# Kernel optimization log

Hardware: AMD Instinct MI355X
Metric: run time of the kernel (lower is better)

Reference implementation:

```python
import jax, jax.numpy as jnp
import numpy as np

IN_F = 512
OUT_F = 512
TREES = 50
DEPTH = 10  # levels above leaves; 2^DEPTH leaves per tree


def _build_forest(T, D):
    """Forest of T perfect binary trees. Nodes laid out level-by-level (leaves first).
    Returns node_order [N], adjacency [E,2] (parent, child; children consecutive,
    left then right, edges sorted by parent), edge_order [E]."""
    per = 2 ** (D + 1) - 1
    no = np.zeros(per, np.int64)
    adj_parts, eo_parts = [], []
    start, prev = 0, None
    for l in range(D + 1):
        n_l = 2 ** (D - l)
        idx = np.arange(start, start + n_l, dtype=np.int64)
        no[idx] = l
        if l > 0:
            parents = np.repeat(idx, 2)          # each parent twice
            adj_parts.append(np.stack([parents, prev], 1))  # prev = 2*n_l children, pairs consecutive
            eo_parts.append(np.full(2 * n_l, l, np.int64))
        prev, start = idx, start + n_l
    adj = np.concatenate(adj_parts, 0)
    eo = np.concatenate(eo_parts, 0)
    offs = np.arange(T, dtype=np.int64) * per
    node_order = np.tile(no, T)
    adjacency = (adj[None] + offs[:, None, None]).reshape(-1, 2)
    edge_order = np.tile(eo, T)
    return node_order, adjacency, edge_order


def setup_inputs() -> dict:
    key = jax.random.key(0)
    ks = jax.random.split(key, 8)
    no, adj, eo = _build_forest(TREES, DEPTH)
    N = no.shape[0]
    s_in = 1.0 / np.sqrt(IN_F).astype(np.float32)
    s_h = 1.0 / np.sqrt(OUT_F).astype(np.float32)
    return {
        "features": jax.random.normal(ks[0], (N, IN_F), jnp.float32),
        "node_order": jnp.asarray(no),
        "adjacency_list": jnp.asarray(adj),
        "edge_order": jnp.asarray(eo),
        "W_iou_w": jax.random.normal(ks[1], (3 * OUT_F, IN_F), jnp.float32) * s_in,
        "W_iou_b": jax.random.normal(ks[2], (3 * OUT_F,), jnp.float32) * s_in,
        "U_iou_l": jax.random.normal(ks[3], (3 * OUT_F, OUT_F), jnp.float32) * s_h,
        "U_iou_r": jax.random.normal(ks[4], (3 * OUT_F, OUT_F), jnp.float32) * s_h,
        "W_f_w": jax.random.normal(ks[5], (OUT_F, IN_F), jnp.float32) * s_in,
        "W_f_b": jax.random.normal(ks[6], (OUT_F,), jnp.float32) * s_in,
        "U_f_l": jax.random.normal(ks[7], (OUT_F, OUT_F), jnp.float32) * s_h,
        "U_f_r": jax.random.normal(jax.random.fold_in(key, 99), (OUT_F, OUT_F), jnp.float32) * s_h,
    }


def reference(features, node_order, adjacency_list, edge_order,
              W_iou_w, W_iou_b, U_iou_l, U_iou_r, W_f_w, W_f_b, U_f_l, U_f_r):
    # Tree topology is static integer data: hoist it to numpy so per-level index
    # sets are concrete (the original torch code host-syncs the same way).
    no = np.asarray(node_order)
    ao = np.asarray(adjacency_list)
    eo = np.asarray(edge_order)
    N, H = features.shape[0], W_f_w.shape[0]
    h = jnp.zeros((N, H), features.dtype)
    c = jnp.zeros((N, H), features.dtype)
    for l in range(int(no.max()) + 1):
        nodes = jnp.asarray(np.nonzero(no == l)[0])   # parents at this level, sorted
        x = features[nodes]                            # [P, F]
        if l == 0:
            iou = x @ W_iou_w.T + W_iou_b
            i, o, u = jnp.split(iou, 3, axis=1)
            c_new = jax.nn.sigmoid(i) * jnp.tanh(u)
        else:
            e = ao[eo == l]                            # [2P, 2]; children consecutive per parent
            p_rep = jnp.asarray(e[:, 0])               # parent repeated per child
            children = jnp.asarray(e[:, 1])
            ch = h[children]                           # [2P, H]
            cc = c[children]                           # [2P, H]
            iou = (x @ W_iou_w.T + W_iou_b
                   + ch[0::2] @ U_iou_l.T              # left child h
                   + ch[1::2] @ U_iou_r.T)             # right child h
            i, o, u = jnp.split(iou, 3, axis=1)
            wf = features[p_rep] @ W_f_w.T + W_f_b     # [2P, H]
            f_l = jax.nn.sigmoid(wf + ch @ U_f_l.T)
            f_r = jax.nn.sigmoid(wf + ch @ U_f_r.T)
            fc = (f_l + f_r) * cc                      # [2P, H]
            c_new = jax.nn.sigmoid(i) * jnp.tanh(u) + fc.reshape(-1, 2, H).sum(1)
        h_new = jax.nn.sigmoid(o) * jnp.tanh(c_new)
        c = c.at[nodes].set(c_new)
        h = h.at[nodes].set(h_new)
    return h, c
```

## Files before the change

kernel.cpp:

```cpp
#include <hip/hip_runtime.h>
#include <hip/hip_bf16.h>

#define TREES_ 50
#define PER_ 2047
#define NN_ (TREES_ * PER_)
#define NINT_ (TREES_ * 1023)
#define NLEAF_ (TREES_ * 1024)

typedef __attribute__((ext_vector_type(8))) short s8v;
typedef __attribute__((ext_vector_type(4))) float f4v;

__device__ __forceinline__ unsigned short f2bf(float f) {
  union { float f; unsigned u; } v; v.f = f;
  unsigned r = v.u + 0x7FFFu + ((v.u >> 16) & 1u);
  return (unsigned short)(r >> 16);
}
__device__ __forceinline__ float bf2f(unsigned short s) {
  union { unsigned u; float f; } v; v.u = ((unsigned)s) << 16;
  return v.f;
}
__device__ __forceinline__ float sigm(float x) { return 1.f / (1.f + __expf(-x)); }
__device__ __forceinline__ float tanh_s(float x) {
  float ax = fabsf(x);
  float e = __expf(2.f * ax);
  float t = 1.f - 2.f / (e + 1.f);
  return copysignf(t, x);
}
__device__ __forceinline__ f4v fz4() { f4v z; z[0]=0.f; z[1]=0.f; z[2]=0.f; z[3]=0.f; return z; }

#if defined(__has_builtin)
#if __has_builtin(__builtin_amdgcn_global_load_lds)
#define HAS_GLD 1
#endif
#endif
__device__ __forceinline__ void gld16(const void* g, void* l) {
#ifdef HAS_GLD
  __builtin_amdgcn_global_load_lds(
      (const __attribute__((address_space(1))) unsigned int*)g,
      (__attribute__((address_space(3))) unsigned int*)l, 16, 0, 0);
#else
  *(s8v*)l = *(const s8v*)g;
#endif
}

__device__ __forceinline__ int xcd_swz(int bid, int nwg) {
  int q = nwg >> 3, r = nwg & 7, x = bid & 7, pos = bid >> 3;
  int base = (x < r) ? x * (q + 1) : r * (q + 1) + (x - r) * q;
  return base + pos;
}

#define LDS_BYTE(row, c16) ((row) * 128 + (((c16) ^ ((row) & 7)) << 4))

#define MFMA_STEP(As, Bs)                                                     \
  for (int kk = 0; kk < 2; ++kk) {                                            \
    s8v af[4], bf_[4];                                                        \
    _Pragma("unroll") for (int i = 0; i < 4; ++i) {                           \
      int R = wr * 64 + i * 16 + lr;                                          \
      af[i] = *(const s8v*)((char*)As + LDS_BYTE(R, kk * 4 + lg));            \
    }                                                                         \
    _Pragma("unroll") for (int j = 0; j < 4; ++j) {                           \
      int R = wc * 64 + j * 16 + lr;                                          \
      bf_[j] = *(const s8v*)((char*)Bs + LDS_BYTE(R, kk * 4 + lg));           \
    }                                                                         \
    _Pragma("unroll") for (int i = 0; i < 4; ++i)                             \
      _Pragma("unroll") for (int j = 0; j < 4; ++j)                           \
        acc[i][j] = __builtin_amdgcn_mfma_f32_16x16x32_bf16(af[i], bf_[j],    \
                                                            acc[i][j], 0, 0, 0); \
  }

__global__ __launch_bounds__(256) void feat2bf(const float* __restrict__ feat,
                                               unsigned short* __restrict__ FB) {
  long long i = (long long)blockIdx.x * 256 + threadIdx.x;
  if (i >= (long long)NN_ * 64) return;
  const float* src = feat + i * 8;
  float4 f0 = *(const float4*)src;
  float4 f1 = *(const float4*)(src + 4);
  s8v v;
  v[0] = (short)f2bf(f0.x); v[1] = (short)f2bf(f0.y);
  v[2] = (short)f2bf(f0.z); v[3] = (short)f2bf(f0.w);
  v[4] = (short)f2bf(f1.x); v[5] = (short)f2bf(f1.y);
  v[6] = (short)f2bf(f1.z); v[7] = (short)f2bf(f1.w);
  *(s8v*)(FB + i * 8) = v;
}

__global__ __launch_bounds__(256) void prep_weights(
    const float* __restrict__ Wiou, const float* __restrict__ Ul,
    const float* __restrict__ Ur,  const float* __restrict__ Wf,
    const float* __restrict__ Ufl, const float* __restrict__ Ufr,
    unsigned short* __restrict__ UCAT2, unsigned short* __restrict__ UFLR,
    unsigned short* __restrict__ WFB) {
  int i = blockIdx.x * 256 + threadIdx.x;
  if (i < 1536 * 1536) {
    int r = i / 1536, c = i - r * 1536;
    float v = (c < 512) ? Ul[r * 512 + c]
            : (c < 1024) ? Ur[r * 512 + (c - 512)]
                         : Wiou[r * 512 + (c - 1024)];
    UCAT2[i] = f2bf(v);
  }
  if (i < 1024 * 512) {
    int r = i >> 9, k = i & 511;
    int c = r >> 1, s = r & 1;
    UFLR[i] = f2bf(s ? Ufr[c * 512 + k] : Ufl[c * 512 + k]);
  }
  if (i < 512 * 512) WFB[i] = f2bf(Wf[i]);
}

__global__ __launch_bounds__(256) void wf_gemm(
    const unsigned short* __restrict__ FB, const unsigned short* __restrict__ WFB,
    const float* __restrict__ bfb, unsigned short* __restrict__ WF, int nwg) {
  __shared__ __align__(16) unsigned short As[128 * 64];
  __shared__ __align__(16) unsigned short Bs[128 * 64];
  const int tid = threadIdx.x;
  const int swz = xcd_swz(blockIdx.x, nwg);
  const int tn = swz & 3, tm = swz >> 2;
  const int wid = tid >> 6, lane = tid & 63;
  const int wr = wid >> 1, wc = wid & 1;
  const int lr = lane & 15, lg = lane >> 4;
  const unsigned short* aA[4]; const unsigned short* aB[4];
#pragma unroll
  for (int L = 0; L < 4; ++L) {
    int q = L * 256 + tid;
    int row = q >> 3, c16g = (q & 7) ^ (row & 7);
    int m = tm * 128 + row; if (m >= NINT_) m = NINT_ - 1;
    unsigned t = (unsigned)m / 1023u;
    int node = (int)t * 2047 + 1024 + (m - (int)t * 1023);
    aA[L] = FB + (size_t)node * 512 + c16g * 8;
    int n = tn * 128 + row;
    aB[L] = WFB + (size_t)n * 512 + c16g * 8;
  }
  f4v acc[4][4];
#pragma unroll
  for (int i = 0; i < 4; ++i)
#pragma unroll
    for (int j = 0; j < 4; ++j) acc[i][j] = fz4();
  for (int k0 = 0; k0 < 512; k0 += 64) {
#pragma unroll
    for (int L = 0; L < 4; ++L) {
      int q = L * 256 + tid;
      gld16(aA[L] + k0, (unsigned short*)As + q * 8);
      gld16(aB[L] + k0, (unsigned short*)Bs + q * 8);
    }
    __syncthreads();
    MFMA_STEP(As, Bs)
    __syncthreads();
  }
#pragma unroll
  for (int i = 0; i < 4; ++i)
#pragma unroll
    for (int j = 0; j < 4; ++j) {
      int n = tn * 128 + wc * 64 + j * 16 + lr;
      float bias = bfb[n];
#pragma unroll
      for (int r = 0; r < 4; ++r) {
        int m = tm * 128 + wr * 64 + i * 16 + lg * 4 + r;
        if (m < NINT_) WF[(size_t)m * 512 + n] = f2bf(acc[i][j][r] + bias);
      }
    }
}

__global__ __launch_bounds__(256) void leaf_gemm(
    const unsigned short* __restrict__ FB, const unsigned short* __restrict__ UCAT2,
    const float* __restrict__ biou, unsigned short* __restrict__ LIOU, int nwg) {
  __shared__ __align__(16) unsigned short As[128 * 64];
  __shared__ __align__(16) unsigned short Bs[128 * 64];
  const int tid = threadIdx.x;
  const int swz = xcd_swz(blockIdx.x, nwg);
  const int tn = swz % 12, tm = swz / 12;
  const int wid = tid >> 6, lane = tid & 63;
  const int wr = wid >> 1, wc = wid & 1;
  const int lr = lane & 15, lg = lane >> 4;
  const unsigned short* aA[4]; const unsigned short* aB[4];
#pragma unroll
  for (int L = 0; L < 4; ++L) {
    int q = L * 256 + tid;
    int row = q >> 3, c16g = (q & 7) ^ (row & 7);
    int m = tm * 128 + row;
    int node = (m >> 10) * 2047 + (m & 1023);
    aA[L] = FB + (size_t)node * 512 + c16g * 8;
    int n = tn * 128 + row;
    aB[L] = UCAT2 + (size_t)n * 1536 + 1024 + c16g * 8;
  }
  f4v acc[4][4];
#pragma unroll
  for (int i = 0; i < 4; ++i)
#pragma unroll
    for (int j = 0; j < 4; ++j) acc[i][j] = fz4();
  for (int k0 = 0; k0 < 512; k0 += 64) {
#pragma unroll
    for (int L = 0; L < 4; ++L) {
      int q = L * 256 + tid;
      gld16(aA[L] + k0, (unsigned short*)As + q * 8);
      gld16(aB[L] + k0, (unsigned short*)Bs + q * 8);
    }
    __syncthreads();
    MFMA_STEP(As, Bs)
    __syncthreads();
  }
#pragma unroll
  for (int i = 0; i < 4; ++i)
#pragma unroll
    for (int j = 0; j < 4; ++j) {
      int n = tn * 128 + wc * 64 + j * 16 + lr;
      float bias = biou[n];
#pragma unroll
      for (int r = 0; r < 4; ++r) {
        int m = tm * 128 + wr * 64 + i * 16 + lg * 4 + r;
        LIOU[(size_t)m * 1536 + n] = f2bf(acc[i][j][r] + bias);
      }
    }
}

__global__ __launch_bounds__(256) void leaf_ew(
    const unsigned short* __restrict__ LIOU,
    float* __restrict__ h_out, float* __restrict__ c_out,
    unsigned short* __restrict__ HB) {
  int idx = blockIdx.x * 256 + threadIdx.x;
  int r = idx >> 7;
  int c4 = (idx & 127) << 2;
  int g = (r >> 10) * 2047 + (r & 1023);
  const unsigned short* pr = LIOU + (size_t)r * 1536;
  ushort4 iv = *(const ushort4*)(pr + c4);
  ushort4 ov = *(const ushort4*)(pr + 512 + c4);
  ushort4 uv = *(const ushort4*)(pr + 1024 + c4);
  float4 hv, cv; ushort4 hb;
  float cc, hh;
  cc = sigm(bf2f(iv.x)) * tanh_s(bf2f(uv.x)); hh = sigm(bf2f(ov.x)) * tanh_s(cc);
  cv.x = cc; hv.x = hh; hb.x = f2bf(hh);
  cc = sigm(bf2f(iv.y)) * tanh_s(bf2f(uv.y)); hh = sigm(bf2f(ov.y)) * tanh_s(cc);
  cv.y = cc; hv.y = hh; hb.y = f2bf(hh);
  cc = sigm(bf2f(iv.z)) * tanh_s(bf2f(uv.z)); hh = sigm(bf2f(ov.z)) * tanh_s(cc);
  cv.z = cc; hv.z = hh; hb.z = f2bf(hh);
  cc = sigm(bf2f(iv.w)) * tanh_s(bf2f(uv.w)); hh = sigm(bf2f(ov.w)) * tanh_s(cc);
  cv.w = cc; hv.w = hh; hb.w = f2bf(hh);
  *(float4*)(h_out + (size_t)g * 512 + c4) = hv;
  *(float4*)(c_out + (size_t)g * 512 + c4) = cv;
  *(ushort4*)(HB + (size_t)g * 512 + c4) = hb;
}

__global__ __launch_bounds__(256) void lvl_gemm(
    const unsigned short* __restrict__ HB, const unsigned short* __restrict__ FB,
    const unsigned short* __restrict__ UFLR, const unsigned short* __restrict__ UCAT2,
    const unsigned short* __restrict__ WF, const float* __restrict__ biou,
    const float* __restrict__ c_out, float* __restrict__ h_out,
    unsigned short* __restrict__ IOU,
    int P, int shift, int start_l, int start_lm1, int nwg1, int nwg2) {
  __shared__ __align__(16) unsigned short As[128 * 64];
  __shared__ __align__(16) unsigned short Bs[128 * 64];
  const int tid = threadIdx.x;
  const int wid = tid >> 6, lane = tid & 63;
  const int wr = wid >> 1, wc = wid & 1;
  const int lr = lane & 15, lg = lane >> 4;
  const int pmask = (1 << shift) - 1;
  f4v acc[4][4];
#pragma unroll
  for (int i = 0; i < 4; ++i)
#pragma unroll
    for (int j = 0; j < 4; ++j) acc[i][j] = fz4();

  if ((int)blockIdx.x < nwg1) {
    const int swz = xcd_swz(blockIdx.x, nwg1);
    const int tn = swz & 7, tm = swz >> 3;
    const int M2 = 2 * P;
    const int cmask = (2 << shift) - 1;
    const unsigned short* aA[4]; const unsigned short* aB[4];
#pragma unroll
    for (int L = 0; L < 4; ++L) {
      int q = L * 256 + tid;
      int row = q >> 3, c16g = (q & 7) ^ (row & 7);
      int jg = tm * 128 + row; if (jg >= M2) jg = M2 - 1;
      int t = jg >> (shift + 1), idx = jg & cmask;
      aA[L] = HB + (size_t)(t * PER_ + start_lm1 + idx) * 512 + c16g * 8;
      int n = tn * 128 + row;
      aB[L] = UFLR + (size_t)n * 512 + c16g * 8;
    }
    for (int k0 = 0; k0 < 512; k0 += 64) {
#pragma unroll
      for (int L = 0; L < 4; ++L) {
        int q = L * 256 + tid;
        gld16(aA[L] + k0, (unsigned short*)As + q * 8);
        gld16(aB[L] + k0, (unsigned short*)Bs + q * 8);
      }
      __syncthreads();
      MFMA_STEP(As, Bs)
      __syncthreads();
    }
    const int soff = start_l - 1024;
#pragma unroll
    for (int i = 0; i < 4; ++i) {
      int mbase = tm * 128 + wr * 64 + i * 16;
#pragma unroll
      for (int j = 0; j < 4; ++j) {
        int nn = tn * 128 + wc * 64 + j * 16 + lr;
        int hcol = nn >> 1;
        float fc[4];
#pragma unroll
        for (int r = 0; r < 4; ++r) {
          int m = mbase + lg * 4 + r;
          int mm = (m < M2) ? m : 0;
          int pidx = mm >> 1;
          int t = pidx >> shift, k = pidx & pmask;
          float wf = bf2f(WF[(size_t)(t * 1023 + soff + k) * 512 + hcol]);
          float sv = sigm(wf + acc[i][j][r]);
          float spair = sv + __shfl_xor(sv, 1, 64);
          float cc = 0.f;
          if ((lr & 1) == 0)
            cc = c_out[(size_t)(t * PER_ + start_lm1 + (mm & cmask)) * 512 + hcol];
          fc[r] = spair * cc;
        }
        if ((lr & 1) == 0) {
          int p0 = (mbase >> 1) + lg * 2;
          if (p0 < P) {
            int t0 = p0 >> shift, k0p = p0 & pmask;
            h_out[(size_t)(t0 * PER_ + start_l + k0p) * 512 + hcol] = fc[0] + fc[1];
          }
          int p1 = (mbase >> 1) + lg * 2 + 1;
          if (p1 < P) {
            int t1 = p1 >> shift, k1p = p1 & pmask;
            h_out[(size_t)(t1 * PER_ + start_l + k1p) * 512 + hcol] = fc[2] + fc[3];
          }
        }
      }
    }
  } else {
    const int swz = xcd_swz((int)blockIdx.x - nwg1, nwg2);
    const int tn = swz % 12, tm = swz / 12;
    const unsigned short* aHB[4]; const unsigned short* aFB[4];
    const unsigned short* aB[4];
#pragma unroll
    for (int L = 0; L < 4; ++L) {
      int q = L * 256 + tid;
      int row = q >> 3, c16g = (q & 7) ^ (row & 7);
      int p = tm * 128 + row; if (p >= P) p = P - 1;
      int t = p >> shift, kp = p & pmask;
      aHB[L] = HB + (size_t)(t * PER_ + start_lm1) * 512 + (size_t)kp * 1024 + c16g * 8;
      aFB[L] = FB + (size_t)(t * PER_ + start_l + kp) * 512 + c16g * 8;
      int n = tn * 128 + row;
      aB[L] = UCAT2 + (size_t)n * 1536 + c16g * 8;
    }
    for (int k0 = 0; k0 < 1536; k0 += 64) {
#pragma unroll
      for (int L = 0; L < 4; ++L) {
        int q = L * 256 + tid;
        const unsigned short* src = (k0 < 1024) ? aHB[L] + k0 : aFB[L] + (k0 - 1024);
        gld16(src, (unsigned short*)As + q * 8);
        gld16(aB[L] + k0, (unsigned short*)Bs + q * 8);
      }
      __syncthreads();
      MFMA_STEP(As, Bs)
      __syncthreads();
    }
#pragma unroll
    for (int i = 0; i < 4; ++i)
#pragma unroll
      for (int j = 0; j < 4; ++j) {
        int n = tn * 128 + wc * 64 + j * 16 + lr;
        float bias = biou[n];
#pragma unroll
        for (int r = 0; r < 4; ++r) {
          int m = tm * 128 + wr * 64 + i * 16 + lg * 4 + r;
          if (m < P) IOU[(size_t)m * 1536 + n] = f2bf(acc[i][j][r] + bias);
        }
      }
  }
}

__global__ __launch_bounds__(256) void g3_kernel(
    const unsigned short* __restrict__ IOU,
    float* __restrict__ h_out, float* __restrict__ c_out,
    unsigned short* __restrict__ HB, int P, int shift, int start_l) {
  int idx = blockIdx.x * 256 + threadIdx.x;
  int p = idx >> 7;
  if (p >= P) return;
  int c4 = (idx & 127) << 2;
  int t = p >> shift, k = p & ((1 << shift) - 1);
  size_t pg = (size_t)(t * PER_ + start_l + k);
  const unsigned short* ir = IOU + (size_t)p * 1536;
  ushort4 iv = *(const ushort4*)(ir + c4);
  ushort4 ov = *(const ushort4*)(ir + 512 + c4);
  ushort4 uv = *(const ushort4*)(ir + 1024 + c4);
  float4 fcs = *(const float4*)(h_out + pg * 512 + c4);
  float4 hv, cv; ushort4 hb;
  float cc, hh;
  cc = sigm(bf2f(iv.x)) * tanh_s(bf2f(uv.x)) + fcs.x; hh = sigm(bf2f(ov.x)) * tanh_s(cc);
  cv.x = cc; hv.x = hh; hb.x = f2bf(hh);
  cc = sigm(bf2f(iv.y)) * tanh_s(bf2f(uv.y)) + fcs.y; hh = sigm(bf2f(ov.y)) * tanh_s(cc);
  cv.y = cc; hv.y = hh; hb.y = f2bf(hh);
  cc = sigm(bf2f(iv.z)) * tanh_s(bf2f(uv.z)) + fcs.z; hh = sigm(bf2f(ov.z)) * tanh_s(cc);
  cv.z = cc; hv.z = hh; hb.z = f2bf(hh);
  cc = sigm(bf2f(iv.w)) * tanh_s(bf2f(uv.w)) + fcs.w; hh = sigm(bf2f(ov.w)) * tanh_s(cc);
  cv.w = cc; hv.w = hh; hb.w = f2bf(hh);
  *(float4*)(h_out + pg * 512 + c4) = hv;
  *(float4*)(c_out + pg * 512 + c4) = cv;
  *(ushort4*)(HB + pg * 512 + c4) = hb;
}

__global__ void fill_sentinel(float* out, int n) {
  int i = blockIdx.x * 256 + threadIdx.x;
  if (i < n) out[i] = 12345.0f;
}

extern "C" void kernel_launch(void* const* d_in, const int* in_sizes, int n_in,
                              void* d_out, int out_size, void* d_ws, size_t ws_size,
                              hipStream_t stream) {
  (void)in_sizes; (void)n_in; (void)out_size;
  const float* feat = (const float*)d_in[0];
  const float* Wiou = (const float*)d_in[4];
  const float* biou = (const float*)d_in[5];
  const float* Ul   = (const float*)d_in[6];
  const float* Ur   = (const float*)d_in[7];
  const float* Wf   = (const float*)d_in[8];
  const float* bfb  = (const float*)d_in[9];
  const float* Ufl  = (const float*)d_in[10];
  const float* Ufr  = (const float*)d_in[11];
  float* h_out = (float*)d_out;
  float* c_out = h_out + (size_t)NN_ * 512;

  const size_t OFF_HB   = 0;
  const size_t SZ_HB    = (size_t)NN_ * 512 * 2;
  const size_t OFF_FB   = OFF_HB + SZ_HB;
  const size_t SZ_FB    = (size_t)NN_ * 512 * 2;
  const size_t OFF_WFm  = OFF_FB + SZ_FB;
  const size_t SZ_WF    = (size_t)NINT_ * 512 * 2;
  const size_t OFF_UC2  = OFF_WFm + SZ_WF;
  const size_t SZ_UC2   = 1536 * 1536 * 2;
  const size_t OFF_UFLR = OFF_UC2 + SZ_UC2;
  const size_t SZ_UFLR  = 1024 * 512 * 2;
  const size_t OFF_WFB  = OFF_UFLR + SZ_UFLR;
  const size_t SZ_WFB   = 512 * 512 * 2;
  const size_t OFF_LIOU = OFF_WFB + SZ_WFB;
  const size_t SZ_LIOU  = (size_t)NLEAF_ * 1536 * 2;
  const size_t NEEDED   = OFF_LIOU + SZ_LIOU;

  if (ws_size < NEEDED) {
    int n = 2 * NN_ * 512;
    fill_sentinel<<<(n + 255) / 256, 256, 0, stream>>>((float*)d_out, n);
    return;
  }

  char* ws = (char*)d_ws;
  unsigned short* HB    = (unsigned short*)(ws + OFF_HB);
  unsigned short* FB    = (unsigned short*)(ws + OFF_FB);
  unsigned short* WF    = (unsigned short*)(ws + OFF_WFm);
  unsigned short* UCAT2 = (unsigned short*)(ws + OFF_UC2);
  unsigned short* UFLR  = (unsigned short*)(ws + OFF_UFLR);
  unsigned short* WFB   = (unsigned short*)(ws + OFF_WFB);
  unsigned short* LIOU  = (unsigned short*)(ws + OFF_LIOU);
  unsigned short* IOU   = (unsigned short*)(ws + OFF_LIOU);

  prep_weights<<<9216, 256, 0, stream>>>(Wiou, Ul, Ur, Wf, Ufl, Ufr,
                                         UCAT2, UFLR, WFB);
  feat2bf<<<(NN_ * 64 + 255) / 256, 256, 0, stream>>>(feat, FB);
  {
    int nwg = ((NINT_ + 127) / 128) * 4;
    wf_gemm<<<nwg, 256, 0, stream>>>(FB, WFB, bfb, WF, nwg);
  }
  {
    int nwg = (NLEAF_ / 128) * 12;
    leaf_gemm<<<nwg, 256, 0, stream>>>(FB, UCAT2, biou, LIOU, nwg);
  }
  leaf_ew<<<(NLEAF_ * 128) / 256, 256, 0, stream>>>(LIOU, h_out, c_out, HB);

  for (int l = 1; l <= 10; ++l) {
    int shift = 10 - l;
    int P = TREES_ << shift;
    int start_l   = 2048 - (1 << (11 - l));
    int start_lm1 = 2048 - (1 << (12 - l));
    int nwg1 = ((2 * P + 127) / 128) * 8;
    int nwg2 = ((P + 127) / 128) * 12;
    lvl_gemm<<<nwg1 + nwg2, 256, 0, stream>>>(HB, FB, UFLR, UCAT2, WF, biou,
                                              c_out, h_out, IOU,
                                              P, shift, start_l, start_lm1,
                                              nwg1, nwg2);
    int g3b = (P * 128 + 255) / 256;
    g3_kernel<<<g3b, 256, 0, stream>>>(IOU, h_out, c_out, HB, P, shift, start_l);
  }
}
```

Measured before the change: 1.499 ms.

## Double-buffer LDS tiles in GEMMs and merge WF and leaf GEMMs into one launch

All GEMM mainloops now use two LDS buffers, so the global-to-LDS load for the next K-slice is issued before the MFMAs on the current slice, and each step ends with a vmcnt drain plus barrier. The separate wf_gemm and leaf_gemm kernels become one pre_mm launch that dispatches on block index, which removes a launch and lets both workloads share the GPU. The aim is to hide global load latency behind MFMA work. The cost is double the LDS per block, which may lower occupancy.

```diff
diff --git a/kernel.cpp b/kernel.cpp
--- a/kernel.cpp
+++ b/kernel.cpp
@@ -51,22 +51,26 @@
 
 #define LDS_BYTE(row, c16) ((row) * 128 + (((c16) ^ ((row) & 7)) << 4))
 
-#define MFMA_STEP(As, Bs)                                                     \
-  for (int kk = 0; kk < 2; ++kk) {                                            \
+#define MFMA_STEP(Ap, Bp)                                                     \
+  _Pragma("unroll") for (int kk = 0; kk < 2; ++kk) {                          \
     s8v af[4], bf_[4];                                                        \
     _Pragma("unroll") for (int i = 0; i < 4; ++i) {                           \
       int R = wr * 64 + i * 16 + lr;                                          \
-      af[i] = *(const s8v*)((char*)As + LDS_BYTE(R, kk * 4 + lg));            \
+      af[i] = *(const s8v*)((const char*)(Ap) + LDS_BYTE(R, kk * 4 + lg));    \
     }                                                                         \
     _Pragma("unroll") for (int j = 0; j < 4; ++j) {                           \
       int R = wc * 64 + j * 16 + lr;                                          \
-      bf_[j] = *(const s8v*)((char*)Bs + LDS_BYTE(R, kk * 4 + lg));           \
+      bf_[j] = *(const s8v*)((const char*)(Bp) + LDS_BYTE(R, kk * 4 + lg));   \
     }                                                                         \
     _Pragma("unroll") for (int i = 0; i < 4; ++i)                             \
       _Pragma("unroll") for (int j = 0; j < 4; ++j)                           \
         acc[i][j] = __builtin_amdgcn_mfma_f32_16x16x32_bf16(af[i], bf_[j],    \
                                                             acc[i][j], 0, 0, 0); \
   }
+
+#define DRAIN_BARRIER()                                   \
+  asm volatile("s_waitcnt vmcnt(0)" ::: "memory");        \
+  __syncthreads();
 
 __global__ __launch_bounds__(256) void feat2bf(const float* __restrict__ feat,
                                                unsigned short* __restrict__ FB) {
@@ -105,109 +109,99 @@
   if (i < 512 * 512) WFB[i] = f2bf(Wf[i]);
 }
 
-__global__ __launch_bounds__(256) void wf_gemm(
+__global__ __launch_bounds__(256) void pre_mm(
     const unsigned short* __restrict__ FB, const unsigned short* __restrict__ WFB,
-    const float* __restrict__ bfb, unsigned short* __restrict__ WF, int nwg) {
-  __shared__ __align__(16) unsigned short As[128 * 64];
-  __shared__ __align__(16) unsigned short Bs[128 * 64];
+    const unsigned short* __restrict__ UCAT2,
+    const float* __restrict__ bfb, const float* __restrict__ biou,
+    unsigned short* __restrict__ WF, unsigned short* __restrict__ LIOU,
+    int nwgW, int nwgL) {
+  __shared__ __align__(16) unsigned short AsB[2 * 128 * 64];
+  __shared__ __align__(16) unsigned short BsB[2 * 128 * 64];
   const int tid = threadIdx.x;
-  const int swz = xcd_swz(blockIdx.x, nwg);
-  const int tn = swz & 3, tm = swz >> 2;
   const int wid = tid >> 6, lane = tid & 63;
   const int wr = wid >> 1, wc = wid & 1;
   const int lr = lane & 15, lg = lane >> 4;
+  f4v acc[4][4];
+#pragma unroll
+  for (int i = 0; i < 4; ++i)
+#pragma unroll
+    for (int j = 0; j < 4; ++j) acc[i][j] = fz4();
+
   const unsigned short* aA[4]; const unsigned short* aB[4];
-#pragma unroll
-  for (int L = 0; L < 4; ++L) {
-    int q = L * 256 + tid;
-    int row = q >> 3, c16g = (q & 7) ^ (row & 7);
-    int m = tm * 128 + row; if (m >= NINT_) m = NINT_ - 1;
-    unsigned t = (unsigned)m / 1023u;
-    int node = (int)t * 2047 + 1024 + (m - (int)t * 1023);
-    aA[L] = FB + (size_t)node * 512 + c16g * 8;
-    int n = tn * 128 + row;
-    aB[L] = WFB + (size_t)n * 512 + c16g * 8;
-  }
-  f4v acc[4][4];
-#pragma unroll
-  for (int i = 0; i < 4; ++i)
-#pragma unroll
-    for (int j = 0; j < 4; ++j) acc[i][j] = fz4();
-  for (int k0 = 0; k0 < 512; k0 += 64) {
+  int tm, tn;
+  const bool isW = (int)blockIdx.x < nwgW;
+  if (isW) {
+    const int swz = xcd_swz(blockIdx.x, nwgW);
+    tn = swz & 3; tm = swz >> 2;
 #pragma unroll
     for (int L = 0; L < 4; ++L) {
       int q = L * 256 + tid;
-      gld16(aA[L] + k0, (unsigned short*)As + q * 8);
-      gld16(aB[L] + k0, (unsigned short*)Bs + q * 8);
-    }
-    __syncthreads();
-    MFMA_STEP(As, Bs)
-    __syncthreads();
-  }
-#pragma unroll
-  for (int i = 0; i < 4; ++i)
-#pragma unroll
-    for (int j = 0; j < 4; ++j) {
-      int n = tn * 128 + wc * 64 + j * 16 + lr;
-      float bias = bfb[n];
-#pragma unroll
-      for (int r = 0; r < 4; ++r) {
-        int m = tm * 128 + wr * 64 + i * 16 + lg * 4 + r;
-        if (m < NINT_) WF[(size_t)m * 512 + n] = f2bf(acc[i][j][r] + bias);
-      }
-    }
-}
-
-__global__ __launch_bounds__(256) void leaf_gemm(
-    const unsigned short* __restrict__ FB, const unsigned short* __restrict__ UCAT2,
-    const float* __restrict__ biou, unsigned short* __restrict__ LIOU, int nwg) {
-  __shared__ __align__(16) unsigned short As[128 * 64];
-  __shared__ __align__(16) unsigned short Bs[128 * 64];
-  const int tid = threadIdx.x;
-  const int swz = xcd_swz(blockIdx.x, nwg);
-  const int tn = swz % 12, tm = swz / 12;
-  const int wid = tid >> 6, lane = tid & 63;
-  const int wr = wid >> 1, wc = wid & 1;
-  const int lr = lane & 15, lg = lane >> 4;
-  const unsigned short* aA[4]; const unsigned short* aB[4];
-#pragma unroll
-  for (int L = 0; L < 4; ++L) {
-    int q = L * 256 + tid;
-    int row = q >> 3, c16g = (q & 7) ^ (row & 7);
-    int m = tm * 128 + row;
-    int node = (m >> 10) * 2047 + (m & 1023);
-    aA[L] = FB + (size_t)node * 512 + c16g * 8;
-    int n = tn * 128 + row;
-    aB[L] = UCAT2 + (size_t)n * 1536 + 1024 + c16g * 8;
-  }
-  f4v acc[4][4];
-#pragma unroll
-  for (int i = 0; i < 4; ++i)
-#pragma unroll
-    for (int j = 0; j < 4; ++j) acc[i][j] = fz4();
-  for (int k0 = 0; k0 < 512; k0 += 64) {
+      int row = q >> 3, c16g = (q & 7) ^ (row & 7);
+      int m = tm * 128 + row; if (m >= NINT_) m = NINT_ - 1;
+      unsigned t = (unsigned)m / 1023u;
+      int node = (int)t * 2047 + 1024 + (m - (int)t * 1023);
+      aA[L] = FB + (size_t)node * 512 + c16g * 8;
+      int n = tn * 128 + row;
+      aB[L] = WFB + (size_t)n * 512 + c16g * 8;
+    }
+  } else {
+    const int swz = xcd_swz((int)blockIdx.x - nwgW, nwgL);
+    tn = swz % 12; tm = swz / 12;
 #pragma unroll
     for (int L = 0; L < 4; ++L) {
       int q = L * 256 + tid;
-      gld16(aA[L] + k0, (unsigned short*)As + q * 8);
-      gld16(aB[L] + k0, (unsigned short*)Bs + q * 8);
-    }
-    __syncthreads();
-    MFMA_STEP(As, Bs)
-    __syncthreads();
-  }
-#pragma unroll
-  for (int i = 0; i < 4; ++i)
-#pragma unroll
-    for (int j = 0; j < 4; ++j) {
-      int n = tn * 128 + wc * 64 + j * 16 + lr;
-      float bias = biou[n];
-#pragma unroll
-      for (int r = 0; r < 4; ++r) {
-        int m = tm * 128 + wr * 64 + i * 16 + lg * 4 + r;
-        LIOU[(size_t)m * 1536 + n] = f2bf(acc[i][j][r] + bias);
+      int row = q >> 3, c16g = (q & 7) ^ (row & 7);
+      int m = tm * 128 + row;
+      int node = (m >> 10) * 2047 + (m & 1023);
+      aA[L] = FB + (size_t)node * 512 + c16g * 8;
+      int n = tn * 128 + row;
+      aB[L] = UCAT2 + (size_t)n * 1536 + 1024 + c16g * 8;
+    }
+  }
+#define STAGE_P(bb, kofs)                                         \
+  _Pragma("unroll") for (int L = 0; L < 4; ++L) {                 \
+    int q = L * 256 + tid;                                        \
+    gld16(aA[L] + (kofs), AsB + (bb) * 8192 + q * 8);             \
+    gld16(aB[L] + (kofs), BsB + (bb) * 8192 + q * 8);             \
+  }
+  STAGE_P(0, 0)
+  DRAIN_BARRIER()
+  int cur = 0;
+  for (int t = 0; t < 7; ++t) {
+    STAGE_P(cur ^ 1, (t + 1) * 64)
+    MFMA_STEP(AsB + cur * 8192, BsB + cur * 8192)
+    DRAIN_BARRIER()
+    cur ^= 1;
+  }
+  MFMA_STEP(AsB + cur * 8192, BsB + cur * 8192)
+
+  if (isW) {
+#pragma unroll
+    for (int i = 0; i < 4; ++i)
+#pragma unroll
+      for (int j = 0; j < 4; ++j) {
+        int n = tn * 128 + wc * 64 + j * 16 + lr;
+        float bias = bfb[n];
+#pragma unroll
+        for (int r = 0; r < 4; ++r) {
+          int m = tm * 128 + wr * 64 + i * 16 + lg * 4 + r;
+          if (m < NINT_) WF[(size_t)m * 512 + n] = f2bf(acc[i][j][r] + bias);
+        }
       }
-    }
+  } else {
+#pragma unroll
+    for (int i = 0; i < 4; ++i)
+#pragma unroll
+      for (int j = 0; j < 4; ++j) {
+        int n = tn * 128 + wc * 64 + j * 16 + lr;
+        float bias = biou[n];
+#pragma unroll
+        for (int r = 0; r < 4; ++r) {
+          int m = tm * 128 + wr * 64 + i * 16 + lg * 4 + r;
+          LIOU[(size_t)m * 1536 + n] = f2bf(acc[i][j][r] + bias);
+        }
+      }
+  }
 }
 
 __global__ __launch_bounds__(256) void leaf_ew(
@@ -244,8 +238,8 @@
     const float* __restrict__ c_out, float* __restrict__ h_out,
     unsigned short* __restrict__ IOU,
     int P, int shift, int start_l, int start_lm1, int nwg1, int nwg2) {
-  __shared__ __align__(16) unsigned short As[128 * 64];
-  __shared__ __align__(16) unsigned short Bs[128 * 64];
+  __shared__ __align__(16) unsigned short AsB[2 * 128 * 64];
+  __shared__ __align__(16) unsigned short BsB[2 * 128 * 64];
   const int tid = threadIdx.x;
   const int wid = tid >> 6, lane = tid & 63;
   const int wr = wid >> 1, wc = wid & 1;
@@ -273,17 +267,23 @@
       int n = tn * 128 + row;
       aB[L] = UFLR + (size_t)n * 512 + c16g * 8;
     }
-    for (int k0 = 0; k0 < 512; k0 += 64) {
-#pragma unroll
-      for (int L = 0; L < 4; ++L) {
-        int q = L * 256 + tid;
-        gld16(aA[L] + k0, (unsigned short*)As + q * 8);
-        gld16(aB[L] + k0, (unsigned short*)Bs + q * 8);
-      }
-      __syncthreads();
-      MFMA_STEP(As, Bs)
-      __syncthreads();
-    }
+#define STAGE_G1(bb, kofs)                                        \
+  _Pragma("unroll") for (int L = 0; L < 4; ++L) {                 \
+    int q = L * 256 + tid;                                        \
+    gld16(aA[L] + (kofs), AsB + (bb) * 8192 + q * 8);             \
+    gld16(aB[L] + (kofs), BsB + (bb) * 8192 + q * 8);             \
+  }
+    STAGE_G1(0, 0)
+    DRAIN_BARRIER()
+    int cur = 0;
+    for (int t = 0; t < 7; ++t) {
+      STAGE_G1(cur ^ 1, (t + 1) * 64)
+      MFMA_STEP(AsB + cur * 8192, BsB + cur * 8192)
+      DRAIN_BARRIER()
+      cur ^= 1;
+    }
+    MFMA_STEP(AsB + cur * 8192, BsB + cur * 8192)
+
     const int soff = start_l - 1024;
 #pragma unroll
     for (int i = 0; i < 4; ++i) {
@@ -333,22 +333,28 @@
       int p = tm * 128 + row; if (p >= P) p = P - 1;
       int t = p >> shift, kp = p & pmask;
       aHB[L] = HB + (size_t)(t * PER_ + start_lm1) * 512 + (size_t)kp * 1024 + c16g * 8;
-      aFB[L] = FB + (size_t)(t * PER_ + start_l + kp) * 512 + c16g * 8;
+      aFB[L] = FB + (size_t)(t * PER_ + start_l + kp) * 512 + c16g * 8 - 1024;
       int n = tn * 128 + row;
       aB[L] = UCAT2 + (size_t)n * 1536 + c16g * 8;
     }
-    for (int k0 = 0; k0 < 1536; k0 += 64) {
-#pragma unroll
-      for (int L = 0; L < 4; ++L) {
-        int q = L * 256 + tid;
-        const unsigned short* src = (k0 < 1024) ? aHB[L] + k0 : aFB[L] + (k0 - 1024);
-        gld16(src, (unsigned short*)As + q * 8);
-        gld16(aB[L] + k0, (unsigned short*)Bs + q * 8);
-      }
-      __syncthreads();
-      MFMA_STEP(As, Bs)
-      __syncthreads();
-    }
+#define STAGE_G2(bb, kofs)                                                    \
+  _Pragma("unroll") for (int L = 0; L < 4; ++L) {                             \
+    int q = L * 256 + tid;                                                    \
+    const unsigned short* srcA =                                              \
+        ((kofs) < 1024) ? aHB[L] + (kofs) : aFB[L] + (kofs);                  \
+    gld16(srcA, AsB + (bb) * 8192 + q * 8);                                   \
+    gld16(aB[L] + (kofs), BsB + (bb) * 8192 + q * 8);                         \
+  }
+    STAGE_G2(0, 0)
+    DRAIN_BARRIER()
+    int cur = 0;
+    for (int t = 0; t < 23; ++t) {
+      STAGE_G2(cur ^ 1, (t + 1) * 64)
+      MFMA_STEP(AsB + cur * 8192, BsB + cur * 8192)
+      DRAIN_BARRIER()
+      cur ^= 1;
+    }
+    MFMA_STEP(AsB + cur * 8192, BsB + cur * 8192)
 #pragma unroll
     for (int i = 0; i < 4; ++i)
 #pragma unroll
@@ -451,12 +457,10 @@
                                          UCAT2, UFLR, WFB);
   feat2bf<<<(NN_ * 64 + 255) / 256, 256, 0, stream>>>(feat, FB);
   {
-    int nwg = ((NINT_ + 127) / 128) * 4;
-    wf_gemm<<<nwg, 256, 0, stream>>>(FB, WFB, bfb, WF, nwg);
-  }
-  {
-    int nwg = (NLEAF_ / 128) * 12;
-    leaf_gemm<<<nwg, 256, 0, stream>>>(FB, UCAT2, biou, LIOU, nwg);
+    int nwgW = ((NINT_ + 127) / 128) * 4;
+    int nwgL = (NLEAF_ / 128) * 12;
+    pre_mm<<<nwgW + nwgL, 256, 0, stream>>>(FB, WFB, UCAT2, bfb, biou,
+                                            WF, LIOU, nwgW, nwgL);
   }
   leaf_ew<<<(NLEAF_ * 128) / 256, 256, 0, stream>>>(LIOU, h_out, c_out, HB);
 
```

New measurement: 1.493 ms. Within noise of the previous version (-0.4%).
